# Kernel tuning notes

Measured on AMD Instinct MI355X. Metric: run time of the kernel, lower is better.

The kernel has to match this reference:

```python
import jax, jax.numpy as jnp
import numpy as np

EPS = 1e-12  # numerical floor inside sqrt for grad stability


def _mean_p2cp(u, v):
    """Mean point-to-closest-point distance.
    u: [..., n, 2] predicted curve points, v: [..., m, 2] target curve points.
    Returns [...] symmetric mean-of-min distances, matching
    MeanP2CPDistance: (min over v per u-point).mean + (min over u per v-point).mean, halved.
    Uses the gram-matrix form of cdist to avoid a [..., n, m, 2] diff tensor.
    """
    u2 = jnp.sum(u * u, axis=-1)                      # [..., n]
    v2 = jnp.sum(v * v, axis=-1)                      # [..., m]
    gram = jnp.einsum('...ik,...jk->...ij', u, v)     # [..., n, m]
    d2 = jnp.maximum(u2[..., :, None] + v2[..., None, :] - 2.0 * gram, 0.0)
    d = jnp.sqrt(d2 + EPS)                            # [..., n, m] pairwise euclidean
    u2v = jnp.min(d, axis=-1).mean(axis=-1)           # for each u point, closest v point
    v2u = jnp.min(d, axis=-2).mean(axis=-1)           # for each v point, closest u point
    return 0.5 * (u2v + v2u)


def setup_inputs() -> dict:
    key = jax.random.key(0)
    k1, k2, k3, k4 = jax.random.split(key, 4)
    bs, seq_len, n_components, n_samples = 8, 512, 12, 128
    outputs = jax.random.normal(k1, (bs, seq_len, n_components), dtype=jnp.float32)
    targets = jax.random.normal(k2, (bs, seq_len, 1, 2, n_samples), dtype=jnp.float32)
    W_dec = jax.random.normal(k3, (n_components, 2 * n_samples), dtype=jnp.float32) * 0.1
    b_dec = jax.random.normal(k4, (2 * n_samples,), dtype=jnp.float32) * 0.01
    return {"outputs": outputs, "targets": targets, "W_dec": W_dec, "b_dec": b_dec}


def reference(outputs, targets, W_dec, b_dec):
    bs, seq_len, n_art, _, n_samples = targets.shape
    # Decode: linear PCA-style decoder n_components -> 2*n_samples
    shapes = outputs @ W_dec + b_dec                       # [bs, seq, 2*n_samples]
    u = shapes.reshape(bs, seq_len, 1, 2, n_samples)       # unsqueeze(2) equivalent
    u = jnp.swapaxes(u, -1, -2)                            # permute(0,1,2,4,3) -> [bs,seq,1,n,2]
    v = jnp.swapaxes(targets, -1, -2)                      # [bs,seq,n_art,n,2]
    p2cp = _mean_p2cp(u, v)                                # [bs,seq,n_art]
    return jnp.mean(p2cp)                                  # reduction='mean'
```

## Files before the change

### kernel.cpp

```cpp
#include <hip/hip_runtime.h>
#include <math.h>
#include <float.h>

#define NCOMP 12
#define NS 128
#define NBS 4096

typedef float f32x2 __attribute__((ext_vector_type(2)));

__global__ __launch_bounds__(256)
void p2cp_block_kernel(const float* __restrict__ outputs,
                       const float* __restrict__ targets,
                       const float* __restrict__ W_dec,
                       const float* __restrict__ b_dec,
                       float* __restrict__ partial) {
    const int bsq = blockIdx.x;
    const int t   = threadIdx.x;

    __shared__ __align__(16) float4 cand4[2][NS / 2];
    __shared__ __align__(8)  float  zz[2 * NS];
    __shared__ float o[NCOMP];
    __shared__ float red[4];

    if (t < NCOMP) o[t] = outputs[bsq * NCOMP + t];

    const float* tb = targets + (size_t)bsq * (2 * NS);
    const float tval = tb[t];
    float vx = 0.0f;
    if (t >= NS) vx = tb[t - NS];
    __syncthreads();

    float x, y;
    int side, idx;
    if (t < NS) {
        side = 0; idx = t;
        x = b_dec[t]; y = b_dec[NS + t];
        #pragma unroll
        for (int k = 0; k < NCOMP; ++k) {
            x = fmaf(o[k], W_dec[k * 256 + t], x);
            y = fmaf(o[k], W_dec[k * 256 + NS + t], y);
        }
    } else {
        side = 1; idx = t - NS;
        x = vx; y = tval;
    }
    float* c4 = reinterpret_cast<float*>(&cand4[side][idx >> 1]);
    c4[(idx & 1)]     = x;
    c4[2 + (idx & 1)] = y;
    zz[t] = fmaf(x, x, y * y);
    __syncthreads();

    const int slice = t & 7;
    const int group = t >> 3;
    const int ownSide = (t < NS) ? 0 : 1;
    const int ownPairBase = (group & 15) * 4;
    const float4* __restrict__ opp4 = cand4[ownSide ^ 1];
    const f32x2*  __restrict__ oppz = reinterpret_cast<const f32x2*>(&zz[(ownSide ^ 1) * NS]);

    f32x2 ab[8];
    float mn[8];
    #pragma unroll
    for (int j = 0; j < 4; ++j) {
        const float4 P = cand4[ownSide][ownPairBase + j];
        f32x2 e0; e0.x = -2.0f * P.x; e0.y = -2.0f * P.z; ab[2 * j]     = e0;
        f32x2 e1; e1.x = -2.0f * P.y; e1.y = -2.0f * P.w; ab[2 * j + 1] = e1;
    }
    #pragma unroll
    for (int k = 0; k < 8; ++k) mn[k] = FLT_MAX;

    #pragma unroll
    for (int i = 0; i < 8; ++i) {
        const int m = slice + 8 * i;
        const float4 q  = opp4[m];
        const f32x2 z2 = oppz[m];
        f32x2 xx; xx.x = q.x; xx.y = q.y;
        f32x2 yy; yy.x = q.z; yy.y = q.w;
        #pragma unroll
        for (int k = 0; k < 8; ++k) {
            f32x2 t1, dd;
            asm("v_pk_fma_f32 %0, %1, %2, %3 op_sel:[1,0,0] op_sel_hi:[1,1,1]"
                : "=v"(t1) : "v"(ab[k]), "v"(yy), "v"(z2));
            asm("v_pk_fma_f32 %0, %1, %2, %3 op_sel:[0,0,0] op_sel_hi:[0,1,1]"
                : "=v"(dd) : "v"(ab[k]), "v"(xx), "v"(t1));
            asm("v_min3_f32 %0, %1, %2, %3"
                : "=v"(mn[k]) : "v"(mn[k]), "v"(dd.x), "v"(dd.y));
        }
    }

    #pragma unroll
    for (int k = 0; k < 8; ++k) {
        mn[k] = fminf(mn[k], __shfl_xor(mn[k], 1));
        mn[k] = fminf(mn[k], __shfl_xor(mn[k], 2));
        mn[k] = fminf(mn[k], __shfl_xor(mn[k], 4));
    }

    float mm = mn[0];
    #pragma unroll
    for (int k = 1; k < 8; ++k) mm = (slice == k) ? mn[k] : mm;
    const float d2 = fmaxf(mm + zz[t], 0.0f);
    float m = sqrtf(d2 + 1e-12f);

    #pragma unroll
    for (int off = 32; off > 0; off >>= 1)
        m += __shfl_down(m, off);
    const int lane = t & 63;
    const int wid  = t >> 6;
    if (lane == 0) red[wid] = m;
    __syncthreads();
    if (t == 0) {
        partial[bsq] = red[0] + red[1] + red[2] + red[3];
    }
}

__global__ __launch_bounds__(256)
void final_reduce_kernel(const float* __restrict__ partial,
                         float* __restrict__ out) {
    const int t = threadIdx.x;
    float s = 0.0f;
    #pragma unroll
    for (int i = 0; i < 16; ++i) s += partial[t + 256 * i];
    #pragma unroll
    for (int off = 32; off > 0; off >>= 1)
        s += __shfl_down(s, off);
    __shared__ float red[4];
    const int lane = t & 63;
    const int wid  = t >> 6;
    if (lane == 0) red[wid] = s;
    __syncthreads();
    if (t == 0) {
        float total = red[0] + red[1] + red[2] + red[3];
        out[0] = total * (1.0f / (256.0f * (float)NBS));
    }
}

extern "C" void kernel_launch(void* const* d_in, const int* in_sizes, int n_in,
                              void* d_out, int out_size, void* d_ws, size_t ws_size,
                              hipStream_t stream) {
    const float* outputs = (const float*)d_in[0];
    const float* targets = (const float*)d_in[1];
    const float* W_dec   = (const float*)d_in[2];
    const float* b_dec   = (const float*)d_in[3];
    float* out = (float*)d_out;
    float* ws  = (float*)d_ws;

    p2cp_block_kernel<<<NBS, 256, 0, stream>>>(outputs, targets, W_dec, b_dec, ws);
    final_reduce_kernel<<<1, 256, 0, stream>>>(ws, out);
}
```

Before: 20.27 us.

## Map each sequence item to one wavefront instead of a whole block

The distance kernel now gives each wavefront one (batch, seq) item and packs four items per block. Each lane decodes four curve coordinates using vectorized float4 loads of W_dec, b_dec and the targets, and swaps halves across lanes with xor-32 shuffles. Each lane then scans all 128 opposite-side points for its four own points. This removes both block-level __syncthreads and the cross-lane min-shuffle stage, and replaces the LDS block reduction with a wave xor-reduction. The cost is a longer serial inner loop per lane and reliance on a manual lgkmcnt wait for intra-wave LDS visibility.

```diff
diff --git a/kernel.cpp b/kernel.cpp
--- a/kernel.cpp
+++ b/kernel.cpp
@@ -5,78 +5,99 @@
 #define NCOMP 12
 #define NS 128
 #define NBS 4096
+#define WPB 4
 
 typedef float f32x2 __attribute__((ext_vector_type(2)));
+typedef float f32x4 __attribute__((ext_vector_type(4)));
+
+__device__ __forceinline__ f32x4 shfl_xor4(f32x4 v, int mask) {
+    f32x4 r;
+    r.x = __shfl_xor(v.x, mask);
+    r.y = __shfl_xor(v.y, mask);
+    r.z = __shfl_xor(v.z, mask);
+    r.w = __shfl_xor(v.w, mask);
+    return r;
+}
 
 __global__ __launch_bounds__(256)
-void p2cp_block_kernel(const float* __restrict__ outputs,
-                       const float* __restrict__ targets,
-                       const float* __restrict__ W_dec,
-                       const float* __restrict__ b_dec,
-                       float* __restrict__ partial) {
-    const int bsq = blockIdx.x;
-    const int t   = threadIdx.x;
+void p2cp_wave_kernel(const float* __restrict__ outputs,
+                      const float* __restrict__ targets,
+                      const float* __restrict__ W_dec,
+                      const float* __restrict__ b_dec,
+                      float* __restrict__ partial) {
+    const int wav  = threadIdx.x >> 6;
+    const int lane = threadIdx.x & 63;
+    const int bsq  = blockIdx.x * WPB + wav;
 
-    __shared__ __align__(16) float4 cand4[2][NS / 2];
-    __shared__ __align__(8)  float  zz[2 * NS];
-    __shared__ float o[NCOMP];
-    __shared__ float red[4];
+    __shared__ __align__(16) f32x4 c4s[WPB][2][NS / 2];
+    __shared__ __align__(16) float zzs[WPB][2][NS];
+    f32x4 (*c4)[NS / 2] = c4s[wav];
+    float (*zw)[NS]     = zzs[wav];
 
-    if (t < NCOMP) o[t] = outputs[bsq * NCOMP + t];
+    const int half = lane >> 5;
+    const int m    = lane & 31;
+
+    const float* ob = outputs + (size_t)bsq * NCOMP;
+    const f32x4 o0 = *reinterpret_cast<const f32x4*>(ob);
+    const f32x4 o1 = *reinterpret_cast<const f32x4*>(ob + 4);
+    const f32x4 o2 = *reinterpret_cast<const f32x4*>(ob + 8);
+
+    f32x4 du = *reinterpret_cast<const f32x4*>(b_dec + 4 * lane);
+    const float* wb = W_dec + 4 * lane;
+    #pragma unroll
+    for (int k = 0; k < 4; ++k)
+        du += o0[k] * *reinterpret_cast<const f32x4*>(wb + (k    ) * 256);
+    #pragma unroll
+    for (int k = 0; k < 4; ++k)
+        du += o1[k] * *reinterpret_cast<const f32x4*>(wb + (k + 4) * 256);
+    #pragma unroll
+    for (int k = 0; k < 4; ++k)
+        du += o2[k] * *reinterpret_cast<const f32x4*>(wb + (k + 8) * 256);
 
     const float* tb = targets + (size_t)bsq * (2 * NS);
-    const float tval = tb[t];
-    float vx = 0.0f;
-    if (t >= NS) vx = tb[t - NS];
-    __syncthreads();
+    const f32x4 dv = *reinterpret_cast<const f32x4*>(tb + 4 * lane);
 
-    float x, y;
-    int side, idx;
-    if (t < NS) {
-        side = 0; idx = t;
-        x = b_dec[t]; y = b_dec[NS + t];
-        #pragma unroll
-        for (int k = 0; k < NCOMP; ++k) {
-            x = fmaf(o[k], W_dec[k * 256 + t], x);
-            y = fmaf(o[k], W_dec[k * 256 + NS + t], y);
-        }
-    } else {
-        side = 1; idx = t - NS;
-        x = vx; y = tval;
+    const f32x4 pu = shfl_xor4(du, 32);
+    const f32x4 pv = shfl_xor4(dv, 32);
+    const f32x4 ox = half ? pv : du;
+    const f32x4 oy = half ? dv : pu;
+    f32x4 zz4;
+    #pragma unroll
+    for (int c = 0; c < 4; ++c) zz4[c] = fmaf(ox[c], ox[c], oy[c] * oy[c]);
+
+    {
+        float* u0 = reinterpret_cast<float*>(&c4[0][2 * m])     + 2 * half;
+        float* u1 = reinterpret_cast<float*>(&c4[0][2 * m + 1]) + 2 * half;
+        float* v0 = reinterpret_cast<float*>(&c4[1][2 * m])     + 2 * half;
+        float* v1 = reinterpret_cast<float*>(&c4[1][2 * m + 1]) + 2 * half;
+        *reinterpret_cast<f32x2*>(u0) = f32x2{du.x, du.y};
+        *reinterpret_cast<f32x2*>(u1) = f32x2{du.z, du.w};
+        *reinterpret_cast<f32x2*>(v0) = f32x2{dv.x, dv.y};
+        *reinterpret_cast<f32x2*>(v1) = f32x2{dv.z, dv.w};
+        *reinterpret_cast<f32x4*>(&zw[half][4 * m]) = zz4;
     }
-    float* c4 = reinterpret_cast<float*>(&cand4[side][idx >> 1]);
-    c4[(idx & 1)]     = x;
-    c4[2 + (idx & 1)] = y;
-    zz[t] = fmaf(x, x, y * y);
-    __syncthreads();
+    asm volatile("s_waitcnt lgkmcnt(0)" ::: "memory");
+    __builtin_amdgcn_sched_barrier(0);
 
-    const int slice = t & 7;
-    const int group = t >> 3;
-    const int ownSide = (t < NS) ? 0 : 1;
-    const int ownPairBase = (group & 15) * 4;
-    const float4* __restrict__ opp4 = cand4[ownSide ^ 1];
-    const f32x2*  __restrict__ oppz = reinterpret_cast<const f32x2*>(&zz[(ownSide ^ 1) * NS]);
+    const f32x4* cp = c4[1 - half];
+    const float* zp = zw[1 - half];
 
-    f32x2 ab[8];
-    float mn[8];
+    f32x2 ab[4];
+    float mn[4];
     #pragma unroll
-    for (int j = 0; j < 4; ++j) {
-        const float4 P = cand4[ownSide][ownPairBase + j];
-        f32x2 e0; e0.x = -2.0f * P.x; e0.y = -2.0f * P.z; ab[2 * j]     = e0;
-        f32x2 e1; e1.x = -2.0f * P.y; e1.y = -2.0f * P.w; ab[2 * j + 1] = e1;
+    for (int k = 0; k < 4; ++k) {
+        ab[k] = f32x2{-2.0f * ox[k], -2.0f * oy[k]};
+        mn[k] = FLT_MAX;
     }
-    #pragma unroll
-    for (int k = 0; k < 8; ++k) mn[k] = FLT_MAX;
 
-    #pragma unroll
-    for (int i = 0; i < 8; ++i) {
-        const int m = slice + 8 * i;
-        const float4 q  = opp4[m];
-        const f32x2 z2 = oppz[m];
+    #pragma unroll 8
+    for (int i = 0; i < NS / 2; ++i) {
+        const f32x4 q  = cp[i];
+        const f32x2 z2 = *reinterpret_cast<const f32x2*>(zp + 2 * i);
         f32x2 xx; xx.x = q.x; xx.y = q.y;
         f32x2 yy; yy.x = q.z; yy.y = q.w;
         #pragma unroll
-        for (int k = 0; k < 8; ++k) {
+        for (int k = 0; k < 4; ++k) {
             f32x2 t1, dd;
             asm("v_pk_fma_f32 %0, %1, %2, %3 op_sel:[1,0,0] op_sel_hi:[1,1,1]"
                 : "=v"(t1) : "v"(ab[k]), "v"(yy), "v"(z2));
@@ -87,29 +108,17 @@
         }
     }
 
+    float s = 0.0f;
     #pragma unroll
-    for (int k = 0; k < 8; ++k) {
-        mn[k] = fminf(mn[k], __shfl_xor(mn[k], 1));
-        mn[k] = fminf(mn[k], __shfl_xor(mn[k], 2));
-        mn[k] = fminf(mn[k], __shfl_xor(mn[k], 4));
+    for (int k = 0; k < 4; ++k) {
+        const float d2 = fmaxf(mn[k] + zz4[k], 0.0f);
+        s += sqrtf(d2 + 1e-12f);
     }
-
-    float mm = mn[0];
-    #pragma unroll
-    for (int k = 1; k < 8; ++k) mm = (slice == k) ? mn[k] : mm;
-    const float d2 = fmaxf(mm + zz[t], 0.0f);
-    float m = sqrtf(d2 + 1e-12f);
-
     #pragma unroll
     for (int off = 32; off > 0; off >>= 1)
-        m += __shfl_down(m, off);
-    const int lane = t & 63;
-    const int wid  = t >> 6;
-    if (lane == 0) red[wid] = m;
-    __syncthreads();
-    if (t == 0) {
-        partial[bsq] = red[0] + red[1] + red[2] + red[3];
-    }
+        s += __shfl_xor(s, off);
+    if (lane == 0)
+        partial[bsq] = s;
 }
 
 __global__ __launch_bounds__(256)
@@ -128,7 +137,7 @@
     if (lane == 0) red[wid] = s;
     __syncthreads();
     if (t == 0) {
-        float total = red[0] + red[1] + red[2] + red[3];
+        const float total = red[0] + red[1] + red[2] + red[3];
         out[0] = total * (1.0f / (256.0f * (float)NBS));
     }
 }
@@ -143,6 +152,6 @@
     float* out = (float*)d_out;
     float* ws  = (float*)d_ws;
 
-    p2cp_block_kernel<<<NBS, 256, 0, stream>>>(outputs, targets, W_dec, b_dec, ws);
+    p2cp_wave_kernel<<<NBS / WPB, 256, 0, stream>>>(outputs, targets, W_dec, b_dec, ws);
     final_reduce_kernel<<<1, 256, 0, stream>>>(ws, out);
 }
```

Result: faster. 17.39 us, median of 2 (-14.2%).
